# Kernel tuning notes

Hardware: AMD Instinct MI355X
Metric: run time of the kernel (lower is better)

The kernel has to match this reference:

```python
import jax, jax.numpy as jnp
import numpy as np

D_MODEL = 512
B, T = 4, 4096


def setup_inputs() -> dict:
    key = jax.random.key(0)
    ks = jax.random.split(key, 5)
    s = 1.0 / np.sqrt(D_MODEL)  # roughly Linear init scale
    return {
        "x": jax.random.normal(ks[0], (B, T, D_MODEL), dtype=jnp.float32),
        "W_q": jax.random.normal(ks[1], (D_MODEL, D_MODEL), dtype=jnp.float32) * s,
        "W_k": jax.random.normal(ks[2], (D_MODEL, D_MODEL), dtype=jnp.float32) * s,
        "W_v": jax.random.normal(ks[3], (D_MODEL, D_MODEL), dtype=jnp.float32) * s,
        "W_o": jax.random.normal(ks[4], (D_MODEL, D_MODEL), dtype=jnp.float32) * s,
    }


def reference(x, W_q, W_k, W_v, W_o):
    # torch nn.Linear(bias=False): y = x @ W.T
    q = jnp.einsum('btd,ed->bte', x, W_q)
    k = jnp.einsum('btd,ed->bte', x, W_k)
    v = jnp.einsum('btd,ed->bte', x, W_v)
    Tq, Tk = q.shape[1], k.shape[1]
    scale = 1.0 / jnp.sqrt(jnp.float32(x.shape[-1]))
    scores = jnp.einsum('bqd,bkd->bqk', q, k) * scale  # [B,T,T]
    causal = jnp.tril(jnp.ones((Tq, Tk), dtype=bool))  # mask triu(diag=1) -> keep lower triangle
    scores = jnp.where(causal[None, :, :], scores, -jnp.inf)
    attn = jax.nn.softmax(scores, axis=-1)
    ctx = jnp.einsum('bqk,bkd->bqd', attn, v)
    out = jnp.einsum('btd,ed->bte', ctx, W_o)
    return out
```

## Files before the change

kernel.cpp:

```cpp
#include <hip/hip_runtime.h>
#include <hip/hip_bf16.h>
#include <math.h>

#define D 512
#define BB 4
#define TT 4096
#define KT 32

typedef __attribute__((ext_vector_type(8))) short short8v;
typedef __attribute__((ext_vector_type(4))) short short4v;
typedef __attribute__((ext_vector_type(4))) float float4v;

__device__ inline short f2bf(float x) {
    __hip_bfloat16 h = __float2bfloat16(x);
    return *reinterpret_cast<short*>(&h);
}
__device__ inline float bf2f(short s) {
    __hip_bfloat16 h = *reinterpret_cast<__hip_bfloat16*>(&s);
    return __bfloat162float(h);
}

__global__ __launch_bounds__(256) void gemm_qkv(
    const float* __restrict__ x,
    const float* __restrict__ Wq, const float* __restrict__ Wk, const float* __restrict__ Wv,
    __hip_bfloat16* __restrict__ q, __hip_bfloat16* __restrict__ k, __hip_bfloat16* __restrict__ vt)
{
    __shared__ short As[64][72];
    __shared__ short Bs[3][64][72];
    __shared__ short Ts[64][66];
    const int tid = threadIdx.x;
    const int m0 = blockIdx.x * 64, n0 = blockIdx.y * 64;
    const int w = tid >> 6, lane = tid & 63, lm = lane & 15, g = lane >> 4;

    float4v acc[3][4];
    #pragma unroll
    for (int z = 0; z < 3; ++z)
        #pragma unroll
        for (int i = 0; i < 4; ++i) acc[z][i] = (float4v){0.f,0.f,0.f,0.f};

    for (int k0 = 0; k0 < 512; k0 += 64) {
        __syncthreads();
        #pragma unroll
        for (int u = 0; u < 4; ++u) {
            int ch = tid + 256*u;
            int r = ch >> 4, c = (ch & 15) * 4;
            float4 xv = *reinterpret_cast<const float4*>(x + (size_t)(m0 + r)*512 + k0 + c);
            short4v sv = { f2bf(xv.x), f2bf(xv.y), f2bf(xv.z), f2bf(xv.w) };
            *reinterpret_cast<short4v*>(&As[r][c]) = sv;
        }
        #pragma unroll
        for (int z = 0; z < 3; ++z) {
            const float* W = (z == 0) ? Wq : (z == 1) ? Wk : Wv;
            #pragma unroll
            for (int u = 0; u < 4; ++u) {
                int ch = tid + 256*u;
                int r = ch >> 4, c = (ch & 15) * 4;
                float4 wv = *reinterpret_cast<const float4*>(W + (size_t)(n0 + r)*512 + k0 + c);
                short4v sv = { f2bf(wv.x), f2bf(wv.y), f2bf(wv.z), f2bf(wv.w) };
                *reinterpret_cast<short4v*>(&Bs[z][r][c]) = sv;
            }
        }
        __syncthreads();
        #pragma unroll
        for (int ks = 0; ks < 2; ++ks) {
            short8v a = *reinterpret_cast<const short8v*>(&As[16*w + lm][ks*32 + 8*g]);
            #pragma unroll
            for (int z = 0; z < 3; ++z)
                #pragma unroll
                for (int nt = 0; nt < 4; ++nt) {
                    short8v bv = *reinterpret_cast<const short8v*>(&Bs[z][16*nt + lm][ks*32 + 8*g]);
                    acc[z][nt] = __builtin_amdgcn_mfma_f32_16x16x32_bf16(a, bv, acc[z][nt], 0, 0, 0);
                }
        }
    }

    #pragma unroll
    for (int z = 0; z < 2; ++z) {
        __hip_bfloat16* C = (z == 0) ? q : k;
        const float alpha = (z == 0) ? 0.044194173824159216f : 1.f;
        #pragma unroll
        for (int nt = 0; nt < 4; ++nt)
            #pragma unroll
            for (int r = 0; r < 4; ++r) {
                int row = m0 + 16*w + 4*g + r;
                int col = n0 + 16*nt + lm;
                C[(size_t)row*512 + col] = __float2bfloat16(acc[z][nt][r] * alpha);
            }
    }

    #pragma unroll
    for (int nt = 0; nt < 4; ++nt)
        #pragma unroll
        for (int r = 0; r < 4; ++r)
            Ts[16*nt + lm][16*w + 4*g + r] = f2bf(acc[2][nt][r]);
    __syncthreads();

    {
        const int dloc = tid >> 2;
        const int qs   = tid & 3;
        const int bb   = m0 >> 12;
        const int tb   = m0 & (TT - 1);
        short tmp[16];
        #pragma unroll
        for (int i = 0; i < 16; ++i) {
            int tp = qs*16 + i;
            int blk = tp & 32;
            int p = tp & 31;
            int tloc = blk + 16*((p & 7) >> 2) + 4*(p >> 3) + (p & 3);
            tmp[i] = Ts[dloc][tloc];
        }
        short* dst = (short*)vt + (size_t)bb*D*TT + (size_t)(n0 + dloc)*TT + tb + qs*16;
        *reinterpret_cast<short8v*>(dst)     = *reinterpret_cast<short8v*>(&tmp[0]);
        *reinterpret_cast<short8v*>(dst + 8) = *reinterpret_cast<short8v*>(&tmp[8]);
    }
}

__global__ __launch_bounds__(512, 1) void attn_split(
    const __hip_bfloat16* __restrict__ qg, const __hip_bfloat16* __restrict__ kg,
    const __hip_bfloat16* __restrict__ vtg,
    __hip_bfloat16* __restrict__ U0, __hip_bfloat16* __restrict__ U1,
    __hip_bfloat16* __restrict__ U2, __hip_bfloat16* __restrict__ U3,
    float* __restrict__ mArr, float* __restrict__ lArr)
{
    __shared__ short Ks[2][KT][512];
    __shared__ short Vs[2][512][32];

    const int tid = threadIdx.x;
    const int w = tid >> 6, lane = tid & 63, lm = lane & 15, g = lane >> 4;
    const int qgp = w;
    const int idx = blockIdx.x;
    const int b  = idx & 3;
    const int u  = idx >> 2;
    const int pr = u >> 2;
    const int s  = u & 3;

    const short* qp = (const short*)qg  + (size_t)b*TT*D;
    const short* kp = (const short*)kg  + (size_t)b*TT*D;
    const short* vp = (const short*)vtg + (size_t)b*D*TT;

    short* Uo = (short*)((s == 0) ? U0 : (s == 1) ? U1 : (s == 2) ? U2 : U3);
    float* mo = mArr + (size_t)s * BB * TT;
    float* lo = lArr + (size_t)s * BB * TT;

    const int vswz = (lane & 3) ^ ((lane >> 3) & 3);

    const short* k0p = &Ks[0][lm][g*8];
    const short* k1p = &Ks[1][lm][g*8];
    const int vcid = g ^ ((lm >> 1) & 3);
    const short* v0p = &Vs[0][lm][vcid*8];
    const short* v1p = &Vs[1][lm][vcid*8];

    #define STAGE_KV(T, BUF) do {                                                  \
        const short* kt_ = kp + (size_t)(T) * KT * D;                              \
        const int ksv_ = (T) * KT;                                                 \
        _Pragma("unroll")                                                          \
        for (int i_ = 0; i_ < 4; ++i_) {                                           \
            int r_ = 4*w + i_;                                                     \
            int c_ = (lane ^ ((r_ & 15) << 2)) & 63;                               \
            __builtin_amdgcn_global_load_lds(                                      \
                (const __attribute__((address_space(1))) void*)(kt_ + (size_t)r_*D + c_*8), \
                (__attribute__((address_space(3))) void*)(&Ks[BUF][r_][0]),        \
                16, 0, 0);                                                         \
        }                                                                          \
        _Pragma("unroll")                                                          \
        for (int i_ = 0; i_ < 4; ++i_) {                                           \
            int d0_ = 64*w + 16*i_;                                                \
            int row_ = d0_ + (lane >> 2);                                          \
            __builtin_amdgcn_global_load_lds(                                      \
                (const __attribute__((address_space(1))) void*)(vp + (size_t)row_*TT + ksv_ + vswz*8), \
                (__attribute__((address_space(3))) void*)(&Vs[BUF][d0_][0]),       \
                16, 0, 0);                                                         \
        }                                                                          \
    } while (0)

    #pragma unroll 1
    for (int phase = 0; phase < 2; ++phase) {
        const int qb = phase ? (31 - pr) : pr;
        const int qbase = qb * 128;
        const int qrow  = qbase + 16*qgp + lm;
        const int t0  = s * (qb + 1);
        const int cnt = qb + 1;

        short8v qf[16];
        #pragma unroll
        for (int ss = 0; ss < 16; ++ss)
            qf[ss] = *reinterpret_cast<const short8v*>(qp + (size_t)qrow*D + 32*ss + 8*g);

        float4v acc[32];
        #pragma unroll
        for (int i = 0; i < 32; ++i) acc[i] = (float4v){0.f,0.f,0.f,0.f};
        float m_r = -INFINITY, l_par = 0.f;

        __syncthreads();
        STAGE_KV(t0, 0);

        for (int i = 0; i < cnt; ++i) {
            const int t = t0 + i;
            const int ks0 = t * KT;
            __syncthreads();
            if (i + 1 < cnt) STAGE_KV(t + 1, (i + 1) & 1);

            const short* kc = (i & 1) ? k1p : k0p;
            const short* vc = (i & 1) ? v1p : v0p;

            float4v s0a = (float4v){0.f,0.f,0.f,0.f}, s0b = (float4v){0.f,0.f,0.f,0.f};
            float4v s1a = (float4v){0.f,0.f,0.f,0.f}, s1b = (float4v){0.f,0.f,0.f,0.f};
            __builtin_amdgcn_s_setprio(1);
            #pragma unroll
            for (int ss = 0; ss < 16; ++ss) {
                int off = (ss ^ lm) << 5;
                short8v a0 = *reinterpret_cast<const short8v*>(kc + off);
                short8v a1 = *reinterpret_cast<const short8v*>(kc + off + 8192);
                if (ss & 1) {
                    s0b = __builtin_amdgcn_mfma_f32_16x16x32_bf16(a0, qf[ss], s0b, 0, 0, 0);
                    s1b = __builtin_amdgcn_mfma_f32_16x16x32_bf16(a1, qf[ss], s1b, 0, 0, 0);
                } else {
                    s0a = __builtin_amdgcn_mfma_f32_16x16x32_bf16(a0, qf[ss], s0a, 0, 0, 0);
                    s1a = __builtin_amdgcn_mfma_f32_16x16x32_bf16(a1, qf[ss], s1a, 0, 0, 0);
                }
            }
            __builtin_amdgcn_s_setprio(0);
            float4v s0, s1;
            #pragma unroll
            for (int r = 0; r < 4; ++r) { s0[r] = s0a[r] + s0b[r]; s1[r] = s1a[r] + s1b[r]; }

            float p[8];
            #pragma unroll
            for (int r = 0; r < 4; ++r) {
                int kj0 = ks0 + 4*g + r;
                p[r]     = (kj0      <= qrow) ? s0[r] : -3.0e38f;
                p[r + 4] = (kj0 + 16 <= qrow) ? s1[r] : -3.0e38f;
            }
            float mx = p[0];
            #pragma unroll
            for (int i2 = 1; i2 < 8; ++i2) mx = fmaxf(mx, p[i2]);

            if (!__all(mx <= m_r + 8.f)) {
                float mrow = fmaxf(mx, __shfl_xor(mx, 16));
                mrow = fmaxf(mrow, __shfl_xor(mrow, 32));
                mrow = fmaxf(mrow, m_r);
                float corr = __expf(m_r - mrow);
                m_r = mrow;
                l_par *= corr;
                #pragma unroll
                for (int dt = 0; dt < 32; ++dt) {
                    acc[dt][0] *= corr; acc[dt][1] *= corr;
                    acc[dt][2] *= corr; acc[dt][3] *= corr;
                }
            }
            #pragma unroll
            for (int i2 = 0; i2 < 8; ++i2) {
                float e = __expf(p[i2] - m_r);
                p[i2] = (p[i2] > -1.0e37f) ? e : 0.f;
                l_par += p[i2];
            }

            short8v pf;
            #pragma unroll
            for (int i2 = 0; i2 < 8; ++i2) pf[i2] = f2bf(p[i2]);

            __builtin_amdgcn_s_setprio(1);
            #pragma unroll
            for (int dt = 0; dt < 32; ++dt) {
                short8v vf = *reinterpret_cast<const short8v*>(vc + dt*512);
                acc[dt] = __builtin_amdgcn_mfma_f32_16x16x32_bf16(vf, pf, acc[dt], 0, 0, 0);
            }
            __builtin_amdgcn_s_setprio(0);
        }

        float l = l_par + __shfl_xor(l_par, 16);
        l += __shfl_xor(l, 32);
        const int orow = qbase + 16*qgp + lm;
        short* up = Uo + (size_t)(b*TT + orow)*D;
        #pragma unroll
        for (int dt = 0; dt < 32; ++dt) {
            short4v o = { f2bf(acc[dt][0]), f2bf(acc[dt][1]),
                          f2bf(acc[dt][2]), f2bf(acc[dt][3]) };
            *reinterpret_cast<short4v*>(up + 16*dt + 4*g) = o;
        }
        if (g == 0) {
            mo[(size_t)b*TT + orow] = m_r;
            lo[(size_t)b*TT + orow] = l;
        }
    }
    #undef STAGE_KV
}

__global__ __launch_bounds__(256) void merge_quads(
    const __hip_bfloat16* __restrict__ U0, const __hip_bfloat16* __restrict__ U1,
    const __hip_bfloat16* __restrict__ U2, const __hip_bfloat16* __restrict__ U3,
    const float* __restrict__ mArr, const float* __restrict__ lArr,
    __hip_bfloat16* __restrict__ ctx)
{
    const int BT = BB * TT;
    const int gidx = blockIdx.x * 256 + threadIdx.x;
    const int row = gidx >> 6;
    const int c = (gidx & 63) * 8;
    float m0 = mArr[row], m1 = mArr[BT + row], m2 = mArr[2*BT + row], m3 = mArr[3*BT + row];
    float ms = fmaxf(fmaxf(m0, m1), fmaxf(m2, m3));
    float w0 = __expf(m0 - ms), w1 = __expf(m1 - ms);
    float w2 = __expf(m2 - ms), w3 = __expf(m3 - ms);
    float l = lArr[row]*w0 + lArr[BT + row]*w1 + lArr[2*BT + row]*w2 + lArr[3*BT + row]*w3;
    float inv = 1.f / l;
    w0 *= inv; w1 *= inv; w2 *= inv; w3 *= inv;
    size_t off = (size_t)row * D + c;
    short8v a = *reinterpret_cast<const short8v*>((const short*)U0 + off);
    short8v b = *reinterpret_cast<const short8v*>((const short*)U1 + off);
    short8v d = *reinterpret_cast<const short8v*>((const short*)U2 + off);
    short8v e = *reinterpret_cast<const short8v*>((const short*)U3 + off);
    short8v o;
    #pragma unroll
    for (int i = 0; i < 8; ++i)
        o[i] = f2bf(bf2f(a[i])*w0 + bf2f(b[i])*w1 + bf2f(d[i])*w2 + bf2f(e[i])*w3);
    *reinterpret_cast<short8v*>((short*)ctx + off) = o;
}

__global__ __launch_bounds__(256) void gemm_out(
    const __hip_bfloat16* __restrict__ Ab, const float* __restrict__ W,
    float* __restrict__ Cf)
{
    __shared__ short As[64][72];
    __shared__ short Bs[64][72];
    const int tid = threadIdx.x;
    const int m0 = blockIdx.x * 64, n0 = blockIdx.y * 64;
    const int w = tid >> 6, lane = tid & 63, lm = lane & 15, g = lane >> 4;
    const short* Ap = (const short*)Ab;

    float4v acc[4];
    #pragma unroll
    for (int i = 0; i < 4; ++i) acc[i] = (float4v){0.f,0.f,0.f,0.f};

    for (int k0 = 0; k0 < 512; k0 += 64) {
        __syncthreads();
        #pragma unroll
        for (int u = 0; u < 2; ++u) {
            int ch = tid + 256*u;
            int r = ch >> 3, c = (ch & 7) * 8;
            *reinterpret_cast<short8v*>(&As[r][c]) =
                *reinterpret_cast<const short8v*>(Ap + (size_t)(m0 + r)*512 + k0 + c);
        }
        #pragma unroll
        for (int u = 0; u < 4; ++u) {
            int ch = tid + 256*u;
            int r = ch >> 4, c = (ch & 15) * 4;
            float4 wv = *reinterpret_cast<const float4*>(W + (size_t)(n0 + r)*512 + k0 + c);
            short4v sv = { f2bf(wv.x), f2bf(wv.y), f2bf(wv.z), f2bf(wv.w) };
            *reinterpret_cast<short4v*>(&Bs[r][c]) = sv;
        }
        __syncthreads();
        #pragma unroll
        for (int ks = 0; ks < 2; ++ks) {
            short8v a = *reinterpret_cast<const short8v*>(&As[16*w + lm][ks*32 + 8*g]);
            #pragma unroll
            for (int nt = 0; nt < 4; ++nt) {
                short8v bv = *reinterpret_cast<const short8v*>(&Bs[16*nt + lm][ks*32 + 8*g]);
                acc[nt] = __builtin_amdgcn_mfma_f32_16x16x32_bf16(a, bv, acc[nt], 0, 0, 0);
            }
        }
    }
    #pragma unroll
    for (int nt = 0; nt < 4; ++nt)
        #pragma unroll
        for (int r = 0; r < 4; ++r) {
            int row = m0 + 16*w + 4*g + r;
            int col = n0 + 16*nt + lm;
            Cf[(size_t)row*512 + col] = acc[nt][r];
        }
}

extern "C" void kernel_launch(void* const* d_in, const int* in_sizes, int n_in,
                              void* d_out, int out_size, void* d_ws, size_t ws_size,
                              hipStream_t stream) {
    const float* x  = (const float*)d_in[0];
    const float* Wq = (const float*)d_in[1];
    const float* Wk = (const float*)d_in[2];
    const float* Wv = (const float*)d_in[3];
    const float* Wo = (const float*)d_in[4];
    float* out = (float*)d_out;

    const size_t n = (size_t)BB * TT * D;
    __hip_bfloat16* qb_  = (__hip_bfloat16*)d_ws;
    __hip_bfloat16* kb_  = qb_ + n;
    __hip_bfloat16* vt_  = kb_ + n;
    __hip_bfloat16* ctxb = vt_ + n;
    __hip_bfloat16* U1   = ctxb + n;
    __hip_bfloat16* U2   = U1 + n;
    __hip_bfloat16* U3   = U2 + n;
    float* mArr = (float*)(U3 + n);
    float* lArr = mArr + (size_t)4 * BB * TT;
    __hip_bfloat16* U0 = (__hip_bfloat16*)out;

    gemm_qkv<<<dim3(256, 8), 256, 0, stream>>>(x, Wq, Wk, Wv, qb_, kb_, vt_);
    attn_split<<<dim3(64 * BB), 512, 0, stream>>>(qb_, kb_, vt_, U0, U1, U2, U3, mArr, lArr);
    merge_quads<<<dim3(BB * TT / 4), 256, 0, stream>>>(U0, U1, U2, U3, mArr, lArr, ctxb);
    gemm_out<<<dim3(256, 8, 1), 256, 0, stream>>>(ctxb, Wo, out);
}
```

Before: 239.5 us.

## Fuse split-attention merge into output projection GEMM with LDS-resident context tile

The separate merge kernel and output GEMM become one kernel. Each 512-thread block merges the four partial attention outputs for 64 rows directly into a swizzled 64x512 LDS tile, then multiplies that tile by all of W_o, with each wave covering 64 output columns. This drops the context round trip through global memory and one launch. In exchange each block converts W_o from fp32 to bf16 straight from global memory without staging, only 256 blocks launch at occupancy 1, and U0 moves out of the output buffer into workspace.

```diff
diff --git a/kernel.cpp b/kernel.cpp
--- a/kernel.cpp
+++ b/kernel.cpp
@@ -286,86 +286,86 @@
     #undef STAGE_KV
 }
 
-__global__ __launch_bounds__(256) void merge_quads(
+__global__ __launch_bounds__(512, 1) void gemm_out_fused(
     const __hip_bfloat16* __restrict__ U0, const __hip_bfloat16* __restrict__ U1,
     const __hip_bfloat16* __restrict__ U2, const __hip_bfloat16* __restrict__ U3,
     const float* __restrict__ mArr, const float* __restrict__ lArr,
-    __hip_bfloat16* __restrict__ ctx)
+    const float* __restrict__ W, float* __restrict__ out)
 {
+    __shared__ short As[64][512];
+    const int tid = threadIdx.x;
+    const int w = tid >> 6, lane = tid & 63, lm = lane & 15, g = lane >> 4;
+    const int m0 = blockIdx.x * 64;
     const int BT = BB * TT;
-    const int gidx = blockIdx.x * 256 + threadIdx.x;
-    const int row = gidx >> 6;
-    const int c = (gidx & 63) * 8;
-    float m0 = mArr[row], m1 = mArr[BT + row], m2 = mArr[2*BT + row], m3 = mArr[3*BT + row];
-    float ms = fmaxf(fmaxf(m0, m1), fmaxf(m2, m3));
-    float w0 = __expf(m0 - ms), w1 = __expf(m1 - ms);
-    float w2 = __expf(m2 - ms), w3 = __expf(m3 - ms);
-    float l = lArr[row]*w0 + lArr[BT + row]*w1 + lArr[2*BT + row]*w2 + lArr[3*BT + row]*w3;
-    float inv = 1.f / l;
-    w0 *= inv; w1 *= inv; w2 *= inv; w3 *= inv;
-    size_t off = (size_t)row * D + c;
-    short8v a = *reinterpret_cast<const short8v*>((const short*)U0 + off);
-    short8v b = *reinterpret_cast<const short8v*>((const short*)U1 + off);
-    short8v d = *reinterpret_cast<const short8v*>((const short*)U2 + off);
-    short8v e = *reinterpret_cast<const short8v*>((const short*)U3 + off);
-    short8v o;
-    #pragma unroll
-    for (int i = 0; i < 8; ++i)
-        o[i] = f2bf(bf2f(a[i])*w0 + bf2f(b[i])*w1 + bf2f(d[i])*w2 + bf2f(e[i])*w3);
-    *reinterpret_cast<short8v*>((short*)ctx + off) = o;
-}
-
-__global__ __launch_bounds__(256) void gemm_out(
-    const __hip_bfloat16* __restrict__ Ab, const float* __restrict__ W,
-    float* __restrict__ Cf)
-{
-    __shared__ short As[64][72];
-    __shared__ short Bs[64][72];
-    const int tid = threadIdx.x;
-    const int m0 = blockIdx.x * 64, n0 = blockIdx.y * 64;
-    const int w = tid >> 6, lane = tid & 63, lm = lane & 15, g = lane >> 4;
-    const short* Ap = (const short*)Ab;
-
-    float4v acc[4];
-    #pragma unroll
-    for (int i = 0; i < 4; ++i) acc[i] = (float4v){0.f,0.f,0.f,0.f};
+
+    {
+        const int row = tid >> 3;
+        const int grow = m0 + row;
+        float ma_ = mArr[grow],        mb_ = mArr[BT + grow];
+        float mc_ = mArr[2*BT + grow], md_ = mArr[3*BT + grow];
+        float ms = fmaxf(fmaxf(ma_, mb_), fmaxf(mc_, md_));
+        float w0 = __expf(ma_ - ms), w1 = __expf(mb_ - ms);
+        float w2 = __expf(mc_ - ms), w3 = __expf(md_ - ms);
+        float l = lArr[grow]*w0 + lArr[BT + grow]*w1 + lArr[2*BT + grow]*w2 + lArr[3*BT + grow]*w3;
+        float inv = 1.f / l;
+        w0 *= inv; w1 *= inv; w2 *= inv; w3 *= inv;
+        const size_t base = (size_t)grow * D;
+        #pragma unroll
+        for (int jc = 0; jc < 8; ++jc) {
+            int j = (tid & 7) * 8 + jc;
+            size_t off = base + (size_t)j * 8;
+            short8v a = *reinterpret_cast<const short8v*>((const short*)U0 + off);
+            short8v b = *reinterpret_cast<const short8v*>((const short*)U1 + off);
+            short8v c = *reinterpret_cast<const short8v*>((const short*)U2 + off);
+            short8v d = *reinterpret_cast<const short8v*>((const short*)U3 + off);
+            short8v o;
+            #pragma unroll
+            for (int i = 0; i < 8; ++i)
+                o[i] = f2bf(bf2f(a[i])*w0 + bf2f(b[i])*w1 + bf2f(c[i])*w2 + bf2f(d[i])*w3);
+            int pj = (j ^ (4 * (row & 15))) & 63;
+            *reinterpret_cast<short8v*>(&As[row][pj * 8]) = o;
+        }
+    }
+    __syncthreads();
+
+    float4v acc[4][4];
+    #pragma unroll
+    for (int rt = 0; rt < 4; ++rt)
+        #pragma unroll
+        for (int nt = 0; nt < 4; ++nt) acc[rt][nt] = (float4v){0.f,0.f,0.f,0.f};
 
     for (int k0 = 0; k0 < 512; k0 += 64) {
-        __syncthreads();
-        #pragma unroll
-        for (int u = 0; u < 2; ++u) {
-            int ch = tid + 256*u;
-            int r = ch >> 3, c = (ch & 7) * 8;
-            *reinterpret_cast<short8v*>(&As[r][c]) =
-                *reinterpret_cast<const short8v*>(Ap + (size_t)(m0 + r)*512 + k0 + c);
-        }
-        #pragma unroll
-        for (int u = 0; u < 4; ++u) {
-            int ch = tid + 256*u;
-            int r = ch >> 4, c = (ch & 15) * 4;
-            float4 wv = *reinterpret_cast<const float4*>(W + (size_t)(n0 + r)*512 + k0 + c);
-            short4v sv = { f2bf(wv.x), f2bf(wv.y), f2bf(wv.z), f2bf(wv.w) };
-            *reinterpret_cast<short4v*>(&Bs[r][c]) = sv;
-        }
-        __syncthreads();
         #pragma unroll
         for (int ks = 0; ks < 2; ++ks) {
-            short8v a = *reinterpret_cast<const short8v*>(&As[16*w + lm][ks*32 + 8*g]);
+            const int j = (((k0 >> 3) + 4*ks + g) ^ (4 * lm)) & 63;
+            short8v a[4];
+            #pragma unroll
+            for (int rt = 0; rt < 4; ++rt)
+                a[rt] = *reinterpret_cast<const short8v*>(&As[16*rt + lm][j * 8]);
             #pragma unroll
             for (int nt = 0; nt < 4; ++nt) {
-                short8v bv = *reinterpret_cast<const short8v*>(&Bs[16*nt + lm][ks*32 + 8*g]);
-                acc[nt] = __builtin_amdgcn_mfma_f32_16x16x32_bf16(a, bv, acc[nt], 0, 0, 0);
-            }
-        }
-    }
-    #pragma unroll
-    for (int nt = 0; nt < 4; ++nt)
-        #pragma unroll
-        for (int r = 0; r < 4; ++r) {
-            int row = m0 + 16*w + 4*g + r;
-            int col = n0 + 16*nt + lm;
-            Cf[(size_t)row*512 + col] = acc[nt][r];
-        }
+                const float* wp = W + (size_t)(64*w + 16*nt + lm)*512 + k0 + 32*ks + 8*g;
+                float4 b0 = *reinterpret_cast<const float4*>(wp);
+                float4 b1 = *reinterpret_cast<const float4*>(wp + 4);
+                short8v bv = { f2bf(b0.x), f2bf(b0.y), f2bf(b0.z), f2bf(b0.w),
+                               f2bf(b1.x), f2bf(b1.y), f2bf(b1.z), f2bf(b1.w) };
+                #pragma unroll
+                for (int rt = 0; rt < 4; ++rt)
+                    acc[rt][nt] = __builtin_amdgcn_mfma_f32_16x16x32_bf16(a[rt], bv, acc[rt][nt], 0, 0, 0);
+            }
+        }
+    }
+
+    #pragma unroll
+    for (int rt = 0; rt < 4; ++rt)
+        #pragma unroll
+        for (int nt = 0; nt < 4; ++nt)
+            #pragma unroll
+            for (int r = 0; r < 4; ++r) {
+                int row = m0 + 16*rt + 4*g + r;
+                int col = 64*w + 16*nt + lm;
+                out[(size_t)row*512 + col] = acc[rt][nt][r];
+            }
 }
 
 extern "C" void kernel_launch(void* const* d_in, const int* in_sizes, int n_in,
@@ -379,19 +379,17 @@
     float* out = (float*)d_out;
 
     const size_t n = (size_t)BB * TT * D;
-    __hip_bfloat16* qb_  = (__hip_bfloat16*)d_ws;
-    __hip_bfloat16* kb_  = qb_ + n;
-    __hip_bfloat16* vt_  = kb_ + n;
-    __hip_bfloat16* ctxb = vt_ + n;
-    __hip_bfloat16* U1   = ctxb + n;
-    __hip_bfloat16* U2   = U1 + n;
-    __hip_bfloat16* U3   = U2 + n;
+    __hip_bfloat16* qb_ = (__hip_bfloat16*)d_ws;
+    __hip_bfloat16* kb_ = qb_ + n;
+    __hip_bfloat16* vt_ = kb_ + n;
+    __hip_bfloat16* U0  = vt_ + n;
+    __hip_bfloat16* U1  = U0 + n;
+    __hip_bfloat16* U2  = U1 + n;
+    __hip_bfloat16* U3  = U2 + n;
     float* mArr = (float*)(U3 + n);
     float* lArr = mArr + (size_t)4 * BB * TT;
-    __hip_bfloat16* U0 = (__hip_bfloat16*)out;
 
     gemm_qkv<<<dim3(256, 8), 256, 0, stream>>>(x, Wq, Wk, Wv, qb_, kb_, vt_);
     attn_split<<<dim3(64 * BB), 512, 0, stream>>>(qb_, kb_, vt_, U0, U1, U2, U3, mArr, lArr);
-    merge_quads<<<dim3(BB * TT / 4), 256, 0, stream>>>(U0, U1, U2, U3, mArr, lArr, ctxb);
-    gemm_out<<<dim3(256, 8, 1), 256, 0, stream>>>(ctxb, Wo, out);
-}
+    gemm_out_fused<<<dim3(256), 512, 0, stream>>>(U0, U1, U2, U3, mArr, lArr, Wo, out);
+}
```

After: 263.9 us. +10.2%, slower.
